# Kernel optimization log

Hardware: AMD Instinct MI355X
Metric: run time of the kernel (lower is better)

The kernel has to match this reference:

```python
import jax, jax.numpy as jnp
import numpy as np
from jax import lax

K = 32            # module k
T = 1             # train_ensemble -> times_sampled
LARGE = 1e10      # LARGE_NUMBER in source
NEG = -1e30       # finite stand-in for -inf (keeps grads NaN-free)


def prefix_logesp(theta, k):
    """Prefix log elementary symmetric polynomials of weights w_i = exp(theta_i).
    theta: (BE, N). Returns F of shape (N+1, BE, k+1) with F[i, b, j] = log e_j(w_1..w_i).
    """
    BE = theta.shape[0]
    init = jnp.concatenate([jnp.zeros((BE, 1), theta.dtype),
                            jnp.full((BE, k), NEG, theta.dtype)], axis=1)

    def step(E, th):
        shifted = jnp.concatenate([jnp.full((BE, 1), NEG, E.dtype), E[:, :-1]], axis=1) + th[:, None]
        Enew = jnp.logaddexp(E, shifted)
        return Enew, Enew

    _, Es = lax.scan(step, init, theta.T)            # Es: (N, BE, k+1)
    return jnp.concatenate([init[None], Es], axis=0)  # (N+1, BE, k+1)


def simple_core(flat, k, times_sampled, key):
    """SIMPLE k-subset layer: exact marginals (log_pr) + conditional-Poisson sampling,
    with straight-through gradient through the marginals (matches the .detach() trick).
    flat: (BE, N) logits. Returns samples (T, BE, N) and marginals (BE, N).
    """
    BE, N = flat.shape
    F = prefix_logesp(flat, k)                       # prefix ESPs, (N+1, BE, k+1)
    B = prefix_logesp(flat[:, ::-1], k)[::-1]        # suffix ESPs: B[i] = ESP of items i..N-1

    # marginal p_i = w_i * e_{k-1}(w \ i) / e_k(w)
    comb = F[:N, :, :k] + B[1:, :, :k][:, :, ::-1]   # (N, BE, k): j + (k-1-j) split
    log_ekm1 = jax.scipy.special.logsumexp(comb, axis=2)  # (N, BE)
    logZ = F[N, :, k]                                # (BE,) log e_k of all weights
    logp = flat.T + log_ekm1 - logZ[None]            # (N, BE)
    marginals = jnp.exp(logp).T                      # (BE, N)

    # exact sequential sampling from the k-subset (conditional Poisson) distribution
    U = jax.random.uniform(key, (N, times_sampled, BE))
    be = jnp.arange(BE)[None, :]

    def samp_step(r, xs):
        th_i, Bi, Bip1, u = xs                       # th_i: (BE,), Bi/Bip1: (BE, k+1), u: (T, BE)
        rm1 = jnp.maximum(r - 1, 0)
        logq = th_i[None, :] + Bip1[be, rm1] - Bi[be, r]
        incl = (u < jnp.exp(jnp.minimum(logq, 0.0))) & (r > 0)
        return r - incl.astype(r.dtype), incl.astype(flat.dtype)

    r0 = jnp.full((times_sampled, BE), k, dtype=jnp.int32)
    _, bits = lax.scan(samp_step, r0, (flat.T, B[:-1], B[1:], U))  # bits: (N, T, BE)
    samples = jnp.transpose(bits, (1, 2, 0))         # (T, BE, N) hard k-hot
    # straight-through: (samples - marginals).detach() + marginals
    samples = lax.stop_gradient(samples - marginals[None]) + marginals[None]
    return samples, marginals


def setup_inputs() -> dict:
    key = jax.random.key(0)
    scores = jax.random.normal(key, (128, 4096, 2), dtype=jnp.float32)
    return {"scores": scores}


def reference(scores):
    bsz, Nmax, ens = scores.shape
    # policy == 'edge_candid'
    flat = jnp.transpose(scores, (0, 2, 1)).reshape(bsz * ens, Nmax)
    target = Nmax
    k = min(K, Nmax)
    N = 2 ** int(np.ceil(np.log2(target)))
    if N > target:  # pad to power of 2 with -LARGE (no-op for Nmax=4096)
        pad = jnp.full((flat.shape[0], N - target), -LARGE, flat.dtype)
        flat = jnp.concatenate([flat, pad], axis=1)
    # logits_activation is None -> pass through
    samples, marginals = simple_core(flat, k, T, jax.random.key(42))
    samples = samples[..., :target]
    marginals = marginals[:, :target]
    new_mask = samples.reshape(T, bsz, ens, Nmax).transpose(0, 1, 3, 2)      # (T, B, Nmax, E)
    new_marginals = marginals.reshape(bsz, ens, Nmax).transpose(0, 2, 1)     # (B, Nmax, E)
    return new_mask, new_marginals
```

## Files before the change

### kernel.cpp

```cpp
#include <hip/hip_runtime.h>
#include <stdint.h>

#pragma clang fp contract(off)

#define BE_C     256
#define N_C      4096
#define K_C      32
#define NEG_C    (-1e30f)
#define OUT_HALF 1048576

__device__ __forceinline__ float xla_exp_neg(float x) {
  const float exp_lo = -88.3762626647949f;
  const float log2ef = 1.44269504088896341f;
  const float c1 = 0.693359375f;
  const float c2 = -2.12194440e-4f;
  const float p0 = 1.9875691500E-4f;
  const float p1 = 1.3981999507E-3f;
  const float p2 = 8.3334519073E-3f;
  const float p3 = 4.1665795894E-2f;
  const float p4 = 1.6666665459E-1f;
  const float p5 = 5.0000001201E-1f;
  float xc = fmaxf(x, exp_lo);
  float fx = floorf(xc * log2ef + 0.5f);
  float tmp = c1 * fx;
  float z = c2 * fx;
  float xx = xc - tmp;
  xx = xx - z;
  z = xx * xx;
  float y = xx * p0 + p1;
  y = y * xx + p2;
  y = y * xx + p3;
  y = y * xx + p4;
  y = y * xx + p5;
  y = y * z + xx;
  y = y + 1.0f;
  int ei = (int)fx;
  float s = __int_as_float((ei + 127) << 23);
  return y * s;
}

__device__ __forceinline__ float xla_log_12(float xin) {
  const float sqrthf = 0.707106781186547524f;
  const float p0 = 7.0376836292E-2f;
  const float p1 = -1.1514610310E-1f;
  const float p2 = 1.1676998740E-1f;
  const float p3 = -1.2420140846E-1f;
  const float p4 = 1.4249322787E-1f;
  const float p5 = -1.6668057665E-1f;
  const float p6 = 2.0000714765E-1f;
  const float p7 = -2.4999993993E-1f;
  const float p8 = 3.3333331174E-1f;
  const float q1 = -2.12194440e-4f;
  const float q2 = 0.693359375f;
  float x = xin;
  unsigned ub = __float_as_uint(x);
  int emm0 = (int)(ub >> 23) - 0x7f;
  float e = 1.0f + (float)emm0;
  x = __uint_as_float((ub & 0x007fffffu) | 0x3f000000u);
  bool mlt = x < sqrthf;
  float tmp = mlt ? x : 0.0f;
  x = x - 1.0f;
  e = e - (mlt ? 1.0f : 0.0f);
  x = x + tmp;
  float x2 = x * x;
  float x3 = x2 * x;
  float y  = x * p0 + p1;
  float y1 = x * p3 + p4;
  float y2 = x * p6 + p7;
  y  = y * x + p2;
  y1 = y1 * x + p5;
  y2 = y2 * x + p8;
  y = y * x3 + y1;
  y = y * x3 + y2;
  y = y * x3;
  y1 = q1 * e;
  float t2 = 0.5f * x2;
  y = y + y1;
  x = x - t2;
  y2 = q2 * e;
  x = x + y;
  x = x + y2;
  return x;
}

__device__ __forceinline__ float xla_log1p_01(float x) {
  float fsmall = ((-0.5f * x) + 1.0f) * x;
  float flarge = xla_log_12(x + 1.0f);
  return (fabsf(x) < 1e-4f) ? fsmall : flarge;
}

__device__ __forceinline__ float xla_logaddexp(float a, float b) {
  float mx = fmaxf(a, b);
  float d = a - b;
  float e = xla_exp_neg(-fabsf(d));
  return mx + xla_log1p_01(e);
}

__device__ __forceinline__ float fast_la(float a, float b) {
  float mx = fmaxf(a, b);
  float d = a - b;
  float e = __expf(-fabsf(d));
  return mx + __logf(1.0f + e);
}

__device__ __forceinline__ float dpp_shr1(float x, float fill) {
  int r = __builtin_amdgcn_update_dpp(__float_as_int(fill), __float_as_int(x),
                                      0x138, 0xF, 0xF, false);
  return __int_as_float(r);
}

__device__ __forceinline__ float readlane_f(float v, int l) {
  return __int_as_float(__builtin_amdgcn_readlane(__float_as_int(v), l));
}

__device__ __forceinline__ unsigned rotl_(unsigned v, int r) {
  return (v << r) | (v >> (32 - r));
}

__device__ __forceinline__ void threefry_0_42(unsigned c0, unsigned c1,
                                              unsigned* o0, unsigned* o1) {
  const unsigned ks0 = 0u, ks1 = 42u, ks2 = 0x1BD11BDAu ^ 0u ^ 42u;
  unsigned x0 = c0 + ks0, x1 = c1 + ks1;
  x0 += x1; x1 = rotl_(x1, 13); x1 ^= x0;
  x0 += x1; x1 = rotl_(x1, 15); x1 ^= x0;
  x0 += x1; x1 = rotl_(x1, 26); x1 ^= x0;
  x0 += x1; x1 = rotl_(x1, 6);  x1 ^= x0;
  x0 += ks1; x1 += ks2 + 1u;
  x0 += x1; x1 = rotl_(x1, 17); x1 ^= x0;
  x0 += x1; x1 = rotl_(x1, 29); x1 ^= x0;
  x0 += x1; x1 = rotl_(x1, 16); x1 ^= x0;
  x0 += x1; x1 = rotl_(x1, 24); x1 ^= x0;
  x0 += ks2; x1 += ks0 + 2u;
  x0 += x1; x1 = rotl_(x1, 13); x1 ^= x0;
  x0 += x1; x1 = rotl_(x1, 15); x1 ^= x0;
  x0 += x1; x1 = rotl_(x1, 26); x1 ^= x0;
  x0 += x1; x1 = rotl_(x1, 6);  x1 ^= x0;
  x0 += ks0; x1 += ks1 + 3u;
  x0 += x1; x1 = rotl_(x1, 17); x1 ^= x0;
  x0 += x1; x1 = rotl_(x1, 29); x1 ^= x0;
  x0 += x1; x1 = rotl_(x1, 16); x1 ^= x0;
  x0 += x1; x1 = rotl_(x1, 24); x1 ^= x0;
  x0 += ks1; x1 += ks2 + 4u;
  x0 += x1; x1 = rotl_(x1, 13); x1 ^= x0;
  x0 += x1; x1 = rotl_(x1, 15); x1 ^= x0;
  x0 += x1; x1 = rotl_(x1, 26); x1 ^= x0;
  x0 += x1; x1 = rotl_(x1, 6);  x1 ^= x0;
  x0 += ks2; x1 += ks0 + 5u;
  *o0 = x0; *o1 = x1;
}

__device__ __forceinline__ float u01_from_idx(unsigned idx) {
  unsigned b0, b1;
  threefry_0_42(0u, idx, &b0, &b1);
  unsigned bits = b0 ^ b1;
  unsigned fb = (bits >> 9) | 0x3f800000u;
  return __uint_as_float(fb) - 1.0f;
}

__device__ __forceinline__ int sw_idx(int row, int col) {
  return row * 32 + ((col + row) & 31);
}

__global__ __launch_bounds__(256)
void EdgeSIMPLEBatched_39298950758997_kernel(const float* __restrict__ scores,
                                             float* __restrict__ out) {
  __shared__ float th_lds[N_C];
  __shared__ float chkB[64 * 32];
  __shared__ float chkF[63 * 32];
  __shared__ float wbuf[4][64 * 32];
  __shared__ float logZ_s;
  __shared__ int   bReady;
  __shared__ int   fReady;
  __shared__ int   claimIdx;

  const int t = threadIdx.x;
  const int w = t >> 6;
  const int lane = t & 63;
  const int b = blockIdx.x;
  const int bi = b >> 1, ens = b & 1;
  const float* srow = scores + bi * (N_C * 2) + ens;
  const int obase = bi * (N_C * 2) + ens;
  const int l31 = lane & 31;

  for (int idx = t; idx < N_C; idx += 256) th_lds[idx] = srow[idx * 2];
  if (t == 0) { bReady = 64; fReady = 0; claimIdx = 0; }
  __syncthreads();

  if (w == 0) {
    float E = (lane == 0) ? 0.0f : NEG_C;
    if (lane < 32) chkB[63 * 32 + lane] = E;
    __threadfence_block();
    if (lane == 0) *(volatile int*)&bReady = 63;
    float thb = th_lds[N_C - 1 - l31];
    float ub  = u01_from_idx((unsigned)((N_C - 1 - l31) * BE_C + b));
    unsigned Wbits = 0u;
#pragma unroll 1
    for (int g = 0; g < 128; ++g) {
      const int nb = (g + 1 < 128) ? g + 1 : g;
      float thb_n = th_lds[N_C - 1 - nb * 32 - l31];
      float ub_n  = u01_from_idx((unsigned)((N_C - 1 - nb * 32 - l31) * BE_C + b));
#pragma unroll 4
      for (int l = 0; l < 32; ++l) {
        float th = readlane_f(thb, l);
        float u  = readlane_f(ub, l);
        float Em1 = dpp_shr1(E, NEG_C);
        float sh = Em1 + th;
        float Enew = xla_logaddexp(E, sh);
        float logq = (th + Em1) - Enew;
        float q = xla_exp_neg(fminf(logq, 0.0f));
        unsigned pb = (u < q) ? 1u : 0u;
        Wbits |= pb << l;
        E = Enew;
      }
      if (lane >= 1 && lane <= 32)
        out[obase + ((127 - g) * 32 + lane - 1) * 2] = __uint_as_float(Wbits);
      Wbits = 0u;
      if ((g & 1) == 1 && g < 127) {
        const int c = ((127 - g) >> 1) - 1;
        if (lane < 32) chkB[c * 32 + lane] = E;
        __threadfence_block();
        if (lane == 0) *(volatile int*)&bReady = c;
      }
      thb = thb_n; ub = ub_n;
    }
    if (lane == 32) logZ_s = E;
    __threadfence_block();
    if (lane == 0) *(volatile int*)&bReady = 0;
  } else if (w == 1) {
    float F = (lane == 0) ? 0.0f : NEG_C;
    float th = th_lds[0];
#pragma unroll 2
    for (int i = 0; i < N_C; ++i) {
      float th_nx = th_lds[(i + 1 < N_C) ? i + 1 : i];
      if ((i & 63) == 0 && i > 0) {
        if (lane < 32) chkF[((i >> 6) - 1) * 32 + lane] = F;
        __threadfence_block();
        if (lane == 0) *(volatile int*)&fReady = (i >> 6);
      }
      float Fm1 = dpp_shr1(F, NEG_C);
      F = fast_la(F, Fm1 + th);
      th = th_nx;
    }
  }

  {
    float* wb = wbuf[w];
    for (;;) {
      int idxv = 0;
      if (lane == 0) idxv = atomicAdd(&claimIdx, 1);
      idxv = __shfl(idxv, 0);
      if (idxv >= 64) break;
      const int c = 63 - idxv;
      while (*(volatile int*)&bReady > c) __builtin_amdgcn_s_sleep(2);
      while (*(volatile int*)&fReady < c) __builtin_amdgcn_s_sleep(2);
      float E2 = chkB[c * 32 + l31];
      if (lane < 32) wb[sw_idx(63, lane)] = E2;
#pragma unroll 1
      for (int ii = 63; ii >= 1; --ii) {
        float th = th_lds[c * 64 + ii];
        float Em1 = dpp_shr1(E2, NEG_C);
        E2 = fast_la(E2, Em1 + th);
        if (lane < 32) wb[sw_idx(ii - 1, lane)] = E2;
      }
      float F2;
      if (c == 0) F2 = (lane == 0) ? 0.0f : NEG_C;
      else        F2 = (lane < 32) ? chkF[(c - 1) * 32 + lane] : NEG_C;
      float th = th_lds[c * 64];
#pragma unroll 2
      for (int ii = 0; ii < 64; ++ii) {
        float th_nx = th_lds[c * 64 + ((ii + 1 < 64) ? ii + 1 : ii)];
        float bbv = wb[sw_idx(ii, (31 - lane) & 31)];
        float comb = F2 + bbv;
        if (lane < 32) wb[sw_idx(ii, lane)] = comb;
        float Fm1 = dpp_shr1(F2, NEG_C);
        F2 = fast_la(F2, Fm1 + th);
        th = th_nx;
      }
      __threadfence_block();
      float cb[32];
#pragma unroll
      for (int jj = 0; jj < 32; ++jj) cb[jj] = wb[sw_idx(lane, jj)];
      float amax = cb[0];
#pragma unroll
      for (int jj = 1; jj < 32; ++jj) amax = fmaxf(amax, cb[jj]);
      float ss = 0.0f;
#pragma unroll
      for (int jj = 0; jj < 32; ++jj) ss += __expf(cb[jj] - amax);
      float thi = th_lds[c * 64 + lane];
      float mraw = thi + (__logf(ss) + amax);
      out[OUT_HALF + obase + (c * 64 + lane) * 2] = mraw;
    }
  }
  __syncthreads();

  {
    const float logZ = logZ_s;
    for (int idx = t; idx < N_C; idx += 256) {
      const int o = OUT_HALF + obase + idx * 2;
      out[o] = __expf(out[o] - logZ);
    }
  }
  __syncthreads();

  if (w == 0) {
    int r = K_C;
    unsigned Wv = 0u;
    if (lane >= 1 && lane <= 32)
      Wv = __float_as_uint(out[obase + (lane - 1) * 2]);
#pragma unroll 1
    for (int g = 127; g >= 0; --g) {
      unsigned Wn = 0u;
      if (g > 0 && lane >= 1 && lane <= 32)
        Wn = __float_as_uint(out[obase + ((128 - g) * 32 + lane - 1) * 2]);
      const int i_l = N_C - 1 - 32 * g - l31;
      float mval = out[OUT_HALF + obase + i_l * 2];
      unsigned inclW = 0u;
#pragma unroll 8
      for (int l = 31; l >= 0; --l) {
        unsigned mm = (unsigned)__builtin_amdgcn_readlane((int)Wv, r);
        unsigned bit = (mm >> l) & 1u;
        inclW |= bit << l;
        r -= (int)bit;
      }
      if (lane < 32) {
        unsigned incl = (inclW >> l31) & 1u;
        float sval = incl ? ((1.0f - mval) + mval) : 0.0f;
        out[obase + i_l * 2] = sval;
      }
      Wv = Wn;
    }
  }
}

extern "C" void kernel_launch(void* const* d_in, const int* in_sizes, int n_in,
                              void* d_out, int out_size, void* d_ws, size_t ws_size,
                              hipStream_t stream) {
  (void)in_sizes; (void)n_in; (void)d_ws; (void)ws_size; (void)out_size;
  const float* scores = (const float*)d_in[0];
  float* out = (float*)d_out;
  EdgeSIMPLEBatched_39298950758997_kernel<<<dim3(BE_C), dim3(256), 0, stream>>>(scores, out);
}
```

Measured before the change: 1.019 ms.

## Offload sampling exp/compare from backward scan wave to a consumer wave via LDS ring

The backward-scan wave no longer computes the random uniforms, the exp of the inclusion log-probability, or the sampling bits. It writes the log-ratio values into a double-buffered LDS ring, and a dedicated wave 2 consumes them to produce the sample bit masks. The aim is to shorten the serial critical path of the backward recurrence. In exchange, the marginal-computation work pool drops from four waves to two (waves 1 and 3), and spin-wait handshakes are added between producer and consumer.

```diff
diff --git a/kernel.cpp b/kernel.cpp
--- a/kernel.cpp
+++ b/kernel.cpp
@@ -167,11 +167,14 @@
   __shared__ float th_lds[N_C];
   __shared__ float chkB[64 * 32];
   __shared__ float chkF[63 * 32];
-  __shared__ float wbuf[4][64 * 32];
+  __shared__ float wtile[2][64 * 32];
+  __shared__ float ring[2][32 * 64];
   __shared__ float logZ_s;
   __shared__ int   bReady;
   __shared__ int   fReady;
   __shared__ int   claimIdx;
+  __shared__ int   ringProd;
+  __shared__ int   consDone;
 
   const int t = threadIdx.x;
   const int w = t >> 6;
@@ -183,7 +186,7 @@
   const int l31 = lane & 31;
 
   for (int idx = t; idx < N_C; idx += 256) th_lds[idx] = srow[idx * 2];
-  if (t == 0) { bReady = 64; fReady = 0; claimIdx = 0; }
+  if (t == 0) { bReady = 64; fReady = 0; claimIdx = 0; ringProd = 0; consDone = 0; }
   __syncthreads();
 
   if (w == 0) {
@@ -192,40 +195,57 @@
     __threadfence_block();
     if (lane == 0) *(volatile int*)&bReady = 63;
     float thb = th_lds[N_C - 1 - l31];
-    float ub  = u01_from_idx((unsigned)((N_C - 1 - l31) * BE_C + b));
-    unsigned Wbits = 0u;
 #pragma unroll 1
     for (int g = 0; g < 128; ++g) {
       const int nb = (g + 1 < 128) ? g + 1 : g;
       float thb_n = th_lds[N_C - 1 - nb * 32 - l31];
-      float ub_n  = u01_from_idx((unsigned)((N_C - 1 - nb * 32 - l31) * BE_C + b));
+      if (g >= 2) {
+        volatile int* cd = &consDone;
+        while (*cd < g - 1) __builtin_amdgcn_s_sleep(1);
+      }
+      float* rg = ring[g & 1];
 #pragma unroll 4
       for (int l = 0; l < 32; ++l) {
         float th = readlane_f(thb, l);
-        float u  = readlane_f(ub, l);
         float Em1 = dpp_shr1(E, NEG_C);
         float sh = Em1 + th;
         float Enew = xla_logaddexp(E, sh);
-        float logq = (th + Em1) - Enew;
-        float q = xla_exp_neg(fminf(logq, 0.0f));
-        unsigned pb = (u < q) ? 1u : 0u;
-        Wbits |= pb << l;
+        rg[l * 64 + lane] = sh - Enew;
         E = Enew;
       }
-      if (lane >= 1 && lane <= 32)
-        out[obase + ((127 - g) * 32 + lane - 1) * 2] = __uint_as_float(Wbits);
-      Wbits = 0u;
+      __threadfence_block();
+      if (lane == 0) *(volatile int*)&ringProd = g + 1;
       if ((g & 1) == 1 && g < 127) {
         const int c = ((127 - g) >> 1) - 1;
         if (lane < 32) chkB[c * 32 + lane] = E;
         __threadfence_block();
         if (lane == 0) *(volatile int*)&bReady = c;
       }
-      thb = thb_n; ub = ub_n;
+      thb = thb_n;
     }
     if (lane == 32) logZ_s = E;
     __threadfence_block();
     if (lane == 0) *(volatile int*)&bReady = 0;
+  } else if (w == 2) {
+#pragma unroll 1
+    for (int g = 0; g < 128; ++g) {
+      float ubv = u01_from_idx((unsigned)((N_C - 1 - g * 32 - l31) * BE_C + b));
+      { volatile int* rp = &ringProd;
+        while (*rp < g + 1) __builtin_amdgcn_s_sleep(1); }
+      float* rg = ring[g & 1];
+      unsigned Wbits = 0u;
+#pragma unroll 8
+      for (int l = 0; l < 32; ++l) {
+        float logq = rg[l * 64 + lane];
+        float u = readlane_f(ubv, l);
+        float q = xla_exp_neg(fminf(logq, 0.0f));
+        Wbits |= ((u < q) ? 1u : 0u) << l;
+      }
+      if (lane >= 1 && lane <= 32)
+        out[obase + ((127 - g) * 32 + lane - 1) * 2] = __uint_as_float(Wbits);
+      __threadfence_block();
+      if (lane == 0) *(volatile int*)&consDone = g + 1;
+    }
   } else if (w == 1) {
     float F = (lane == 0) ? 0.0f : NEG_C;
     float th = th_lds[0];
@@ -243,8 +263,8 @@
     }
   }
 
-  {
-    float* wb = wbuf[w];
+  if (w == 1 || w == 3) {
+    float* wb = wtile[(w == 1) ? 0 : 1];
     for (;;) {
       int idxv = 0;
       if (lane == 0) idxv = atomicAdd(&claimIdx, 1);
```

After: 1.045 ms. 1.03x slower.
